# Kernel tuning notes

Measured on AMD Instinct MI355X. Metric: run time of the kernel, lower is better.

Reference implementation:

```python
import jax, jax.numpy as jnp
import numpy as np

N, S, R, M, C, CZ = 1, 128, 256, 256, 32, 128


def setup_inputs() -> dict:
    key = jax.random.key(0)
    k1, k2, k3, k4 = jax.random.split(key, 4)
    return {
        "msa_repr": jax.random.normal(k1, (N, S, R, M), dtype=jnp.float32) * 0.1,
        "left_w": jax.random.normal(k2, (M, C), dtype=jnp.float32) * 0.02,
        "right_w": jax.random.normal(k3, (M, C), dtype=jnp.float32) * 0.02,
        "out_w": jax.random.normal(k4, (C * C, CZ), dtype=jnp.float32) * 0.02,
    }


def reference(msa_repr, left_w, right_w, out_w):
    # msa_repr: [N,S,R,M]
    n, s, r, m = msa_repr.shape
    c = left_w.shape[1]
    # opm_projection: [N,S,R,M] @ [M,C] -> [N,S,R,C]
    left = jnp.einsum('nsrm,mc->nsrc', msa_repr, left_w)
    right = jnp.einsum('nsrm,mc->nsrc', msa_repr, right_w)
    # outer product summed over MSA dim s: [N,R,T,C,C]
    # (torch: a=left.transpose(-2,-3) -> [N,R,S,C]; einsum '...bac,...dae->...bdce')
    outer = jnp.einsum('nsrc,nste->nrtce', left, right).reshape(n, r, r, c * c)
    # project to pair channel: [N,R,T,C*C] @ [C*C,CZ] -> [N,R,T,CZ]
    return jnp.matmul(outer, out_w)
```

## Files before the change

### kernel.cpp

```cpp
#include <hip/hip_runtime.h>
#include <stdint.h>

#define S_DIM 128
#define R_DIM 256
#define M_DIM 256
#define C_DIM 32
#define CZ_DIM 128
#define K2_DIM 1024

typedef _Float16 f16;
typedef _Float16 f16x4 __attribute__((ext_vector_type(4)));
typedef _Float16 f16x8 __attribute__((ext_vector_type(8)));
typedef float f32x4 __attribute__((ext_vector_type(4)));
typedef float f32x16 __attribute__((ext_vector_type(16)));

__global__ void prep_kernel(const float* __restrict__ lw, const float* __restrict__ rw,
                            const float* __restrict__ ow,
                            f16* __restrict__ wt_l, f16* __restrict__ wt_r,
                            f16* __restrict__ wt2) {
    int idx = blockIdx.x * blockDim.x + threadIdx.x;
    int stride = gridDim.x * blockDim.x;
    for (int i = idx; i < CZ_DIM * K2_DIM; i += stride) {
        int cz = i >> 10, k2 = i & 1023;
        int c = k2 >> 5, e = k2 & 31;
        int k2p = ((e >> 2) << 7) + (c << 2) + (e & 3);
        int ntile = cz >> 5, l31 = cz & 31;
        int kk = k2p >> 4, q5 = (k2p >> 3) & 1, j = k2p & 7;
        wt2[(ntile * 64 + kk) * 512 + (l31 * 2 + q5) * 8 + j] = (f16)ow[k2 * CZ_DIM + cz];
    }
    for (int i = idx; i < C_DIM * M_DIM; i += stride) {
        int c = i >> 8, m = i & 255;
        wt_l[i] = (f16)lw[m * C_DIM + c];
        wt_r[i] = (f16)rw[m * C_DIM + c];
    }
}

__global__ __launch_bounds__(256, 4)
void proj_kernel(const float* __restrict__ msa, const f16* __restrict__ wt_l,
                 const f16* __restrict__ wt_r,
                 f16* __restrict__ left_t, f16* __restrict__ rt2) {
    int bid = blockIdx.x;
    int r  = bid >> 1;
    int s0 = (bid & 1) << 6;
    int tid = threadIdx.x;
    int w = tid >> 6;
    int lane = tid & 63;
    int q = lane >> 4, li = lane & 15;

    int s_col = s0 + w * 16 + li;
    const f32x4* bp = (const f32x4*)(msa + ((size_t)s_col * R_DIM + r) * M_DIM + q * 8);

    f32x4 b[16];
#pragma unroll
    for (int ks = 0; ks < 8; ks++) { b[2 * ks] = bp[ks * 8]; b[2 * ks + 1] = bp[ks * 8 + 1]; }

    f32x4 aL0 = {0,0,0,0}, aL1 = {0,0,0,0}, aR0 = {0,0,0,0}, aR1 = {0,0,0,0};
#pragma unroll
    for (int ks = 0; ks < 8; ks++) {
        f16x8 bf;
#pragma unroll
        for (int u = 0; u < 4; u++) { bf[u] = (f16)b[2*ks][u]; bf[4 + u] = (f16)b[2*ks+1][u]; }
        const f16* a0 = wt_l + li * M_DIM + ks * 32 + q * 8;
        const f16* a1 = wt_r + li * M_DIM + ks * 32 + q * 8;
        f16x8 al0 = *(const f16x8*)(a0);
        f16x8 al1 = *(const f16x8*)(a0 + 16 * M_DIM);
        f16x8 ar0 = *(const f16x8*)(a1);
        f16x8 ar1 = *(const f16x8*)(a1 + 16 * M_DIM);
        aL0 = __builtin_amdgcn_mfma_f32_16x16x32_f16(al0, bf, aL0, 0, 0, 0);
        aL1 = __builtin_amdgcn_mfma_f32_16x16x32_f16(al1, bf, aL1, 0, 0, 0);
        aR0 = __builtin_amdgcn_mfma_f32_16x16x32_f16(ar0, bf, aR0, 0, 0, 0);
        aR1 = __builtin_amdgcn_mfma_f32_16x16x32_f16(ar1, bf, aR1, 0, 0, 0);
    }
    int ks_s = s_col >> 4, q5_s = (s_col >> 3) & 1, j_s = s_col & 7;
    int sbase = (r * 8 + ks_s) * 512 + q5_s * 8 + j_s;
#pragma unroll
    for (int reg = 0; reg < 4; reg++) {
        int c0 = q * 4 + reg;
        left_t[(r * C_DIM + c0) * S_DIM + s_col]      = (f16)aL0[reg];
        left_t[(r * C_DIM + c0 + 16) * S_DIM + s_col] = (f16)aL1[reg];
        rt2[sbase + c0 * 16]        = (f16)aR0[reg];
        rt2[sbase + (c0 + 16) * 16] = (f16)aR1[reg];
    }
}

__global__ __launch_bounds__(512, 4)
void fuse_kernel(const f16* __restrict__ left_t, const f16* __restrict__ rt2,
                 const f16* __restrict__ wt2, float* __restrict__ out) {
    __shared__ __align__(16) char lds[65536];
    f16* Ls = (f16*)lds;

    int bid = blockIdx.x;
    int br = bid >> 6, bt = bid & 63;
    int tid = threadIdx.x;
    int w = tid >> 6, lane = tid & 63;
    int q5 = lane >> 5, l31 = lane & 31, lx = lane & 15;

    const f16* Lg = left_t + (size_t)br * 32768;

    int t_tile = w & 3, rg4 = w >> 2;
    int g = bt * 4 + t_tile;
    const f16* ap = rt2 + (size_t)g * 4096 + (l31 * 2 + q5) * 8;
    f16x8 afr[8];
#pragma unroll
    for (int ks = 0; ks < 8; ks++) afr[ks] = *(const f16x8*)(ap + ks * 512);

#pragma unroll
    for (int it = 0; it < 8; it++) {
        int G = it * 512 + tid, row = G >> 4, ch = G & 15;
        f16x8 v = *(const f16x8*)(Lg + G * 8);
        *(f16x8*)(Ls + row * 128 + ((ch ^ (row & 15)) << 3)) = v;
    }
    __syncthreads();

    f32x16 acc[4] = {};
#pragma unroll
    for (int i = 0; i < 4; i++) {
        const f16* bbase = Ls + ((rg4 * 4 + i) * 32 + l31) * 128;
#pragma unroll
        for (int ks = 0; ks < 8; ks++) {
            f16x8 bfr = *(const f16x8*)(bbase + (((2 * ks + q5) ^ lx) << 3));
            acc[i] = __builtin_amdgcn_mfma_f32_32x32x16_f16(afr[ks], bfr, acc[i], 0, 0, 0);
        }
    }

    int ntile = w & 3, kh = w >> 2;
    const f16* wbase = wt2 + (size_t)(ntile * 64 + kh * 32) * 512 + (l31 * 2 + q5) * 8;
    f16x8 wfc[4], wfn[4];
#pragma unroll
    for (int u = 0; u < 4; u++) wfc[u] = *(const f16x8*)(wbase + u * 512);

    __syncthreads();

    int chc = l31 >> 1, bsub = 8 * (l31 & 1);
#pragma unroll
    for (int i = 0; i < 4; i++) {
        int p = (rg4 * 4 + i) * 4 + t_tile;
        char* prow = lds + p * 2048;
#pragma unroll
        for (int rg = 0; rg < 4; rg++) {
            int ch = (2 * rg + q5) * 16 + chc;
            int phys = (ch + p) & 127;
            f16x4 h = {(f16)acc[i][4 * rg], (f16)acc[i][4 * rg + 1],
                       (f16)acc[i][4 * rg + 2], (f16)acc[i][4 * rg + 3]};
            *(f16x4*)(prow + phys * 16 + bsub) = h;
        }
    }
    __syncthreads();

    const char* lbase = lds + l31 * 2048;
    f32x16 accA = {}, accB = {};
#pragma unroll 1
    for (int gg = 0; gg < 8; gg++) {
        int k0 = gg * 4;
        if (gg < 7) {
#pragma unroll
            for (int u = 0; u < 4; u++)
                wfn[u] = *(const f16x8*)(wbase + (k0 + 4 + u) * 512);
        }
        f16x8 af[4];
#pragma unroll
        for (int u = 0; u < 4; u++) {
            int ks2 = kh * 32 + k0 + u;
            int phys = (2 * ks2 + q5 + l31) & 127;
            af[u] = *(const f16x8*)(lbase + phys * 16);
        }
        accA = __builtin_amdgcn_mfma_f32_32x32x16_f16(af[0], wfc[0], accA, 0, 0, 0);
        accB = __builtin_amdgcn_mfma_f32_32x32x16_f16(af[1], wfc[1], accB, 0, 0, 0);
        accA = __builtin_amdgcn_mfma_f32_32x32x16_f16(af[2], wfc[2], accA, 0, 0, 0);
        accB = __builtin_amdgcn_mfma_f32_32x32x16_f16(af[3], wfc[3], accB, 0, 0, 0);
#pragma unroll
        for (int u = 0; u < 4; u++) wfc[u] = wfn[u];
    }
    f32x16 acc2;
#pragma unroll
    for (int v = 0; v < 16; v++) acc2[v] = accA[v] + accB[v];
    __syncthreads();

    if (w >= 4) {
        char* rb = lds + (w - 4) * 4096 + lane * 64;
#pragma unroll
        for (int u = 0; u < 4; u++) {
            f32x4 part = {acc2[4 * u], acc2[4 * u + 1], acc2[4 * u + 2], acc2[4 * u + 3]};
            *(f32x4*)(rb + u * 16) = part;
        }
    }
    __syncthreads();
    if (w < 4) {
        const char* rb = lds + w * 4096 + lane * 64;
#pragma unroll
        for (int u = 0; u < 4; u++) {
            f32x4 part = *(const f32x4*)(rb + u * 16);
#pragma unroll
            for (int v = 0; v < 4; v++) acc2[4 * u + v] += part[v];
        }
        int r0 = br * 8, t0 = bt * 4, cz = w * 32 + l31;
#pragma unroll
        for (int reg = 0; reg < 16; reg++) {
            int p = (reg & 3) + 8 * (reg >> 2) + 4 * q5;
            out[((size_t)((r0 + (p >> 2)) * R_DIM + t0 + (p & 3))) * CZ_DIM + cz] = acc2[reg];
        }
    }
}

extern "C" void kernel_launch(void* const* d_in, const int* in_sizes, int n_in,
                              void* d_out, int out_size, void* d_ws, size_t ws_size,
                              hipStream_t stream) {
    const float* msa = (const float*)d_in[0];
    const float* lw  = (const float*)d_in[1];
    const float* rw  = (const float*)d_in[2];
    const float* ow  = (const float*)d_in[3];
    char* ws = (char*)d_ws;
    f16* left_t = (f16*)(ws);
    f16* rt2    = (f16*)(ws + (size_t)2 * 1024 * 1024);
    f16* wt2    = (f16*)(ws + (size_t)4 * 1024 * 1024);
    f16* wt_l   = (f16*)(ws + (size_t)4 * 1024 * 1024 + 262144);
    f16* wt_r   = (f16*)(ws + (size_t)4 * 1024 * 1024 + 262144 + 16384);
    float* out  = (float*)d_out;

    prep_kernel<<<dim3(256), dim3(256), 0, stream>>>(lw, rw, ow, wt_l, wt_r, wt2);
    proj_kernel<<<dim3(512), dim3(256), 0, stream>>>(msa, wt_l, wt_r, left_t, rt2);
    fuse_kernel<<<dim3(2048), dim3(512), 0, stream>>>(left_t, rt2, wt2, out);
}
```

Before: 144.9 us.

## Split fused outer-product stage into two c-halves with separate LDS regions

The fuse kernel now handles the left channel dimension in two halves of 16. Each half stages its own left slice into a 32 KB LDS region, computes the outer product, writes it back as fp16, and runs the output projection before the second half starts. The weight layout in prep is reordered to match this split. The aim is to cut live accumulator registers (2 tiles instead of 4) and give the scheduler independent work across halves. The cost is more barriers and a more complex indexing scheme.

```diff
diff --git a/kernel.cpp b/kernel.cpp
--- a/kernel.cpp
+++ b/kernel.cpp
@@ -13,6 +13,8 @@
 typedef _Float16 f16x8 __attribute__((ext_vector_type(8)));
 typedef float f32x4 __attribute__((ext_vector_type(4)));
 typedef float f32x16 __attribute__((ext_vector_type(16)));
+
+#define MFMA32(a, b, c) __builtin_amdgcn_mfma_f32_32x32x16_f16(a, b, c, 0, 0, 0)
 
 __global__ void prep_kernel(const float* __restrict__ lw, const float* __restrict__ rw,
                             const float* __restrict__ ow,
@@ -23,10 +25,12 @@
     for (int i = idx; i < CZ_DIM * K2_DIM; i += stride) {
         int cz = i >> 10, k2 = i & 1023;
         int c = k2 >> 5, e = k2 & 31;
-        int k2p = ((e >> 2) << 7) + (c << 2) + (e & 3);
+        int X = c >> 4, cl = c & 15;
+        int k2ph = ((e >> 2) << 6) + (cl << 2) + (e & 3);
+        int kk = k2ph >> 4, q5 = (k2ph >> 3) & 1, j = k2ph & 7;
         int ntile = cz >> 5, l31 = cz & 31;
-        int kk = k2p >> 4, q5 = (k2p >> 3) & 1, j = k2p & 7;
-        wt2[(ntile * 64 + kk) * 512 + (l31 * 2 + q5) * 8 + j] = (f16)ow[k2 * CZ_DIM + cz];
+        wt2[(((X * 4 + ntile) * 32) + kk) * 512 + (l31 * 2 + q5) * 8 + j] =
+            (f16)ow[k2 * CZ_DIM + cz];
     }
     for (int i = idx; i < C_DIM * M_DIM; i += stride) {
         int c = i >> 8, m = i & 255;
@@ -83,97 +87,113 @@
     }
 }
 
+__device__ __forceinline__ void phase1_half(const f16* stg, const f16x8* afr,
+                                            int rg4, int l31, int q5, int lx,
+                                            f32x16* acc) {
+#pragma unroll
+    for (int i = 0; i < 2; i++) {
+        const f16* bbase = stg + ((rg4 * 2 + i) * 32 + l31) * 128;
+#pragma unroll
+        for (int ks = 0; ks < 8; ks++) {
+            f16x8 bfr = *(const f16x8*)(bbase + (((2 * ks + q5) ^ lx) << 3));
+            acc[i] = MFMA32(afr[ks], bfr, acc[i]);
+        }
+    }
+}
+
+__device__ __forceinline__ void phase2_half(char* region, const f32x16* acc,
+                                            int rg4, int t_tile, int l31, int q5) {
+    int cl = l31 & 15, r_hi = l31 >> 4;
+#pragma unroll
+    for (int i = 0; i < 2; i++) {
+        int p = ((rg4 * 2 + i) * 2 + r_hi) * 4 + t_tile;
+        char* prow = region + p * 1024;
+#pragma unroll
+        for (int rg = 0; rg < 4; rg++) {
+            int chunk = (2 * rg + q5) * 8 + (cl >> 1);
+            int phys = (chunk + p) & 63;
+            f16x4 h = {(f16)acc[i][4 * rg], (f16)acc[i][4 * rg + 1],
+                       (f16)acc[i][4 * rg + 2], (f16)acc[i][4 * rg + 3]};
+            *(f16x4*)(prow + phys * 16 + (cl & 1) * 8) = h;
+        }
+    }
+}
+
+__device__ __forceinline__ void stage2_half(const char* region, const f16* wbaseX,
+                                            const f16x8* wpre, int l31, int q5, int kh,
+                                            f32x16& accP, f32x16& accQ) {
+    const char* lbase = region + l31 * 1024;
+#pragma unroll
+    for (int kk = 0; kk < 16; kk++) {
+        f16x8 wf = (kk < 4) ? wpre[kk & 3] : *(const f16x8*)(wbaseX + kk * 512);
+        int s = kh * 16 + kk;
+        int phys = ((s * 2 + q5) + l31) & 63;
+        f16x8 af = *(const f16x8*)(lbase + phys * 16);
+        if (kk & 1) accQ = MFMA32(af, wf, accQ);
+        else        accP = MFMA32(af, wf, accP);
+    }
+}
+
 __global__ __launch_bounds__(512, 4)
 void fuse_kernel(const f16* __restrict__ left_t, const f16* __restrict__ rt2,
                  const f16* __restrict__ wt2, float* __restrict__ out) {
     __shared__ __align__(16) char lds[65536];
-    f16* Ls = (f16*)lds;
 
     int bid = blockIdx.x;
     int br = bid >> 6, bt = bid & 63;
     int tid = threadIdx.x;
     int w = tid >> 6, lane = tid & 63;
     int q5 = lane >> 5, l31 = lane & 31, lx = lane & 15;
-
-    const f16* Lg = left_t + (size_t)br * 32768;
-
     int t_tile = w & 3, rg4 = w >> 2;
+    int ntile = w & 3, kh = w >> 2;
+    size_t rc0 = (size_t)br * 256;
+
     int g = bt * 4 + t_tile;
     const f16* ap = rt2 + (size_t)g * 4096 + (l31 * 2 + q5) * 8;
     f16x8 afr[8];
 #pragma unroll
     for (int ks = 0; ks < 8; ks++) afr[ks] = *(const f16x8*)(ap + ks * 512);
 
+    const f16* wbaseA = wt2 + (size_t)((0 * 4 + ntile) * 32 + kh * 16) * 512 + (l31 * 2 + q5) * 8;
+    const f16* wbaseB = wt2 + (size_t)((1 * 4 + ntile) * 32 + kh * 16) * 512 + (l31 * 2 + q5) * 8;
+    f16x8 wpreA[4];
+#pragma unroll
+    for (int u = 0; u < 4; u++) wpreA[u] = *(const f16x8*)(wbaseA + u * 512);
+
 #pragma unroll
     for (int it = 0; it < 8; it++) {
-        int G = it * 512 + tid, row = G >> 4, ch = G & 15;
-        f16x8 v = *(const f16x8*)(Lg + G * 8);
-        *(f16x8*)(Ls + row * 128 + ((ch ^ (row & 15)) << 3)) = v;
-    }
-    __syncthreads();
-
-    f32x16 acc[4] = {};
-#pragma unroll
-    for (int i = 0; i < 4; i++) {
-        const f16* bbase = Ls + ((rg4 * 4 + i) * 32 + l31) * 128;
-#pragma unroll
-        for (int ks = 0; ks < 8; ks++) {
-            f16x8 bfr = *(const f16x8*)(bbase + (((2 * ks + q5) ^ lx) << 3));
-            acc[i] = __builtin_amdgcn_mfma_f32_32x32x16_f16(afr[ks], bfr, acc[i], 0, 0, 0);
-        }
-    }
-
-    int ntile = w & 3, kh = w >> 2;
-    const f16* wbase = wt2 + (size_t)(ntile * 64 + kh * 32) * 512 + (l31 * 2 + q5) * 8;
-    f16x8 wfc[4], wfn[4];
-#pragma unroll
-    for (int u = 0; u < 4; u++) wfc[u] = *(const f16x8*)(wbase + u * 512);
-
-    __syncthreads();
-
-    int chc = l31 >> 1, bsub = 8 * (l31 & 1);
-#pragma unroll
-    for (int i = 0; i < 4; i++) {
-        int p = (rg4 * 4 + i) * 4 + t_tile;
-        char* prow = lds + p * 2048;
-#pragma unroll
-        for (int rg = 0; rg < 4; rg++) {
-            int ch = (2 * rg + q5) * 16 + chc;
-            int phys = (ch + p) & 127;
-            f16x4 h = {(f16)acc[i][4 * rg], (f16)acc[i][4 * rg + 1],
-                       (f16)acc[i][4 * rg + 2], (f16)acc[i][4 * rg + 3]};
-            *(f16x4*)(prow + phys * 16 + bsub) = h;
-        }
-    }
-    __syncthreads();
-
-    const char* lbase = lds + l31 * 2048;
-    f32x16 accA = {}, accB = {};
-#pragma unroll 1
-    for (int gg = 0; gg < 8; gg++) {
-        int k0 = gg * 4;
-        if (gg < 7) {
-#pragma unroll
-            for (int u = 0; u < 4; u++)
-                wfn[u] = *(const f16x8*)(wbase + (k0 + 4 + u) * 512);
-        }
-        f16x8 af[4];
-#pragma unroll
-        for (int u = 0; u < 4; u++) {
-            int ks2 = kh * 32 + k0 + u;
-            int phys = (2 * ks2 + q5 + l31) & 127;
-            af[u] = *(const f16x8*)(lbase + phys * 16);
-        }
-        accA = __builtin_amdgcn_mfma_f32_32x32x16_f16(af[0], wfc[0], accA, 0, 0, 0);
-        accB = __builtin_amdgcn_mfma_f32_32x32x16_f16(af[1], wfc[1], accB, 0, 0, 0);
-        accA = __builtin_amdgcn_mfma_f32_32x32x16_f16(af[2], wfc[2], accA, 0, 0, 0);
-        accB = __builtin_amdgcn_mfma_f32_32x32x16_f16(af[3], wfc[3], accB, 0, 0, 0);
-#pragma unroll
-        for (int u = 0; u < 4; u++) wfc[u] = wfn[u];
-    }
+        int G = it * 512 + tid;
+        int X = G >> 11, h = G & 2047;
+        int hrow = h >> 4, ch = h & 15;
+        int r = hrow >> 4, cl = hrow & 15;
+        f16x8 v = *(const f16x8*)(left_t + (rc0 + r * 32 + cl + X * 16) * 128 + ch * 8);
+        *(f16x8*)(lds + X * 32768 + hrow * 256 + ((ch ^ (hrow & 15)) << 4)) = v;
+    }
+    __syncthreads();
+
+    f32x16 accA[2] = {};
+    phase1_half((const f16*)lds, afr, rg4, l31, q5, lx, accA);
+    __syncthreads();
+    phase2_half(lds, accA, rg4, t_tile, l31, q5);
+    __syncthreads();
+
+    f32x16 accP = {}, accQ = {};
+    stage2_half(lds, wbaseA, wpreA, l31, q5, kh, accP, accQ);
+
+    f16x8 wpreB[4];
+#pragma unroll
+    for (int u = 0; u < 4; u++) wpreB[u] = *(const f16x8*)(wbaseB + u * 512);
+
+    f32x16 accB[2] = {};
+    phase1_half((const f16*)(lds + 32768), afr, rg4, l31, q5, lx, accB);
+    __syncthreads();
+    phase2_half(lds + 32768, accB, rg4, t_tile, l31, q5);
+    __syncthreads();
+    stage2_half(lds + 32768, wbaseB, wpreB, l31, q5, kh, accP, accQ);
+
     f32x16 acc2;
 #pragma unroll
-    for (int v = 0; v < 16; v++) acc2[v] = accA[v] + accB[v];
+    for (int v = 0; v < 16; v++) acc2[v] = accP[v] + accQ[v];
     __syncthreads();
 
     if (w >= 4) {
```

Measured after the change: 144.6 us. Within noise of the previous version (-0.2%).
